# Performance work log

Measured on AMD Instinct MI355X. Metric: run time of the kernel, lower is better.

The kernel has to match this reference:

```python
import jax, jax.numpy as jnp
import numpy as np

Q_MAX = 127.0  # 2**(8-1) - 1

def _quant_per_tensor_absmax(t):
    # scale = clamp(absmax, 1e-5) / 127 ; q = round(t / scale)
    scale = jnp.maximum(jnp.max(jnp.abs(t)), 1e-5) / Q_MAX
    q = jnp.round(t / scale)
    return q, scale

def setup_inputs() -> dict:
    key = jax.random.key(0)
    k1, k2, k3 = jax.random.split(key, 3)
    B, S, IN, OUT = 4, 2048, 4096, 4096
    x = jax.random.normal(k1, (B, S, IN), dtype=jnp.float32)
    weight = jax.random.normal(k2, (OUT, IN), dtype=jnp.float32)
    bias = jax.random.normal(k3, (1, OUT), dtype=jnp.float32)
    return {"x": x, "weight": weight, "bias": bias}

def reference(x, weight, bias):
    # per-tensor weight quantization (done at from_float time in the original)
    q_w, s_w = _quant_per_tensor_absmax(weight)   # q_w: [OUT, IN] integer-valued
    # per-tensor activation quantization (forward path)
    q_x, s_x = _quant_per_tensor_absmax(x)        # q_x: [B, S, IN] integer-valued
    # int8 GEMM (simulated in fp32: values are small integers) + fused dequant
    y = jnp.einsum('bsi,oi->bso', q_x, q_w)       # [B, S, OUT]
    y = y * (s_x * s_w) + bias                    # dequant scale + bias
    return y
```

## Files before the change

### kernel.cpp

```cpp
#include <hip/hip_runtime.h>
#include <hip/hip_bf16.h>
#include <stdint.h>

#define M_DIM 8192
#define N_DIM 4096
#define K_DIM 4096

typedef int i32x4 __attribute__((ext_vector_type(4)));

#define NB_X 2048
#define NB_W 1024
#define NB_TOT (NB_X + NB_W)

__global__ void w8a8_absmax_kernel(const float* __restrict__ x,
                                   const float* __restrict__ w,
                                   float* __restrict__ partials) {
    int b = blockIdx.x;
    const float4* p;
    int n4, bi, nb;
    if (b < NB_X) { p = (const float4*)x; n4 = (M_DIM * K_DIM) / 4; bi = b;        nb = NB_X; }
    else          { p = (const float4*)w; n4 = (N_DIM * K_DIM) / 4; bi = b - NB_X; nb = NB_W; }

    float m = 0.f;
    int stride = nb * 256;
    for (int i = bi * 256 + threadIdx.x; i < n4; i += stride) {
        float4 v = p[i];
        m = fmaxf(m, fmaxf(fmaxf(fabsf(v.x), fabsf(v.y)), fmaxf(fabsf(v.z), fabsf(v.w))));
    }
    #pragma unroll
    for (int o = 32; o > 0; o >>= 1)
        m = fmaxf(m, __shfl_xor(m, o, 64));

    __shared__ float red[4];
    if ((threadIdx.x & 63) == 0) red[threadIdx.x >> 6] = m;
    __syncthreads();
    if (threadIdx.x == 0)
        partials[b] = fmaxf(fmaxf(red[0], red[1]), fmaxf(red[2], red[3]));
}

__global__ void w8a8_finalize_kernel(const float* __restrict__ partials,
                                     float* __restrict__ finals) {
    int base = (blockIdx.x == 0) ? 0 : NB_X;
    int n    = (blockIdx.x == 0) ? NB_X : NB_W;
    float m = 0.f;
    for (int i = threadIdx.x; i < n; i += 256)
        m = fmaxf(m, partials[base + i]);
    #pragma unroll
    for (int o = 32; o > 0; o >>= 1)
        m = fmaxf(m, __shfl_xor(m, o, 64));
    __shared__ float red[4];
    if ((threadIdx.x & 63) == 0) red[threadIdx.x >> 6] = m;
    __syncthreads();
    if (threadIdx.x == 0) {
        m = fmaxf(fmaxf(red[0], red[1]), fmaxf(red[2], red[3]));
        finals[blockIdx.x] = fmaxf(m, 1e-5f) / 127.0f;
    }
}

__global__ void w8a8_quant_kernel(const float* __restrict__ x,
                                  const float* __restrict__ w,
                                  unsigned* __restrict__ qx,
                                  unsigned* __restrict__ qw,
                                  const float* __restrict__ finals) {
    int b = blockIdx.x;
    const float4* in4;
    unsigned* outq;
    int n4, bi, nb;
    float scale;
    if (b < NB_X) { in4 = (const float4*)x; outq = qx; n4 = (M_DIM * K_DIM) / 4; bi = b;        nb = NB_X; scale = finals[0]; }
    else          { in4 = (const float4*)w; outq = qw; n4 = (N_DIM * K_DIM) / 4; bi = b - NB_X; nb = NB_W; scale = finals[1]; }

    int stride = nb * 256;
    for (int i = bi * 256 + threadIdx.x; i < n4; i += stride) {
        float4 v = in4[i];
        int q0 = (int)rintf(v.x / scale);
        int q1 = (int)rintf(v.y / scale);
        int q2 = (int)rintf(v.z / scale);
        int q3 = (int)rintf(v.w / scale);
        outq[i] = (unsigned)(q0 & 0xff) | ((unsigned)(q1 & 0xff) << 8) |
                  ((unsigned)(q2 & 0xff) << 16) | ((unsigned)(q3 & 0xff) << 24);
    }
}

#define BM 256
#define BN 256
#define BK 128
#define NT (K_DIM / BK)
#define NTN (N_DIM / BN)
#define LDS_BUF 65536

#define STAGE_A(BUF, MH, KT) do {                                              \
    _Pragma("unroll")                                                          \
    for (int r_ = 0; r_ < 2; ++r_)                                             \
        __builtin_amdgcn_global_load_lds(                                      \
            (const __attribute__((address_space(1))) void*)(a_base + (size_t)((KT) + goffA[MH][r_])), \
            (__attribute__((address_space(3))) void*)(lds + (BUF)*LDS_BUF + (MH)*16384 + ldst[r_]),   \
            16, 0, 0);                                                         \
} while (0)

#define STAGE_B(BUF, NH, KT) do {                                              \
    _Pragma("unroll")                                                          \
    for (int r_ = 0; r_ < 2; ++r_)                                             \
        __builtin_amdgcn_global_load_lds(                                      \
            (const __attribute__((address_space(1))) void*)(b_base + (size_t)((KT) + goffB[NH][r_])), \
            (__attribute__((address_space(3))) void*)(lds + (BUF)*LDS_BUF + 32768 + (NH)*16384 + ldst[r_]), \
            16, 0, 0);                                                         \
} while (0)

#define LOAD_A(BUF, MH) do {                                                   \
    _Pragma("unroll")                                                          \
    for (int m4_ = 0; m4_ < 4; ++m4_) {                                        \
        aF[m4_][0] = *(const i32x4*)(lds + (BUF)*LDS_BUF + (MH)*16384 + laneA + m4_*2048 + koff[0]); \
        aF[m4_][1] = *(const i32x4*)(lds + (BUF)*LDS_BUF + (MH)*16384 + laneA + m4_*2048 + koff[1]); \
    }                                                                          \
} while (0)

#define LOAD_B(BUF, NH) do {                                                   \
    _Pragma("unroll")                                                          \
    for (int n1_ = 0; n1_ < 2; ++n1_) {                                        \
        bF[n1_][0] = *(const i32x4*)(lds + (BUF)*LDS_BUF + 32768 + (NH)*16384 + laneB + n1_*2048 + koff[0]); \
        bF[n1_][1] = *(const i32x4*)(lds + (BUF)*LDS_BUF + 32768 + (NH)*16384 + laneB + n1_*2048 + koff[1]); \
    }                                                                          \
} while (0)

#define MMA(MH, NH) do {                                                       \
    __builtin_amdgcn_s_setprio(1);                                             \
    _Pragma("unroll")                                                          \
    for (int m4_ = 0; m4_ < 4; ++m4_) {                                        \
        _Pragma("unroll")                                                      \
        for (int n1_ = 0; n1_ < 2; ++n1_) {                                    \
            i32x4 c_ = acc[(MH)*4 + m4_][(NH)*2 + n1_];                        \
            c_ = __builtin_amdgcn_mfma_i32_16x16x64_i8(aF[m4_][0], bF[n1_][0], c_, 0, 0, 0); \
            c_ = __builtin_amdgcn_mfma_i32_16x16x64_i8(aF[m4_][1], bF[n1_][1], c_, 0, 0, 0); \
            acc[(MH)*4 + m4_][(NH)*2 + n1_] = c_;                              \
        }                                                                      \
    }                                                                          \
    __builtin_amdgcn_s_setprio(0);                                             \
} while (0)

#define BAR() __builtin_amdgcn_s_barrier()
#define VMW8() asm volatile("s_waitcnt vmcnt(8)" ::: "memory")

#define TILE_BODY(BUF, KT2) do {                                               \
    LOAD_A(BUF, 0); LOAD_B(BUF, 0);                         \
    BAR(); MMA(0, 0); BAR();                                                   \
    LOAD_A(BUF, 1);                                         \
    BAR(); MMA(1, 0); BAR();                                                   \
    LOAD_B(BUF, 1);                                         \
    STAGE_B(BUF, 0, KT2);                              \
    BAR(); MMA(1, 1); BAR();                                                   \
    LOAD_A(BUF, 0);                                         \
    STAGE_A(BUF, 1, KT2);                              \
    STAGE_B(BUF, 1, KT2);                              \
    BAR(); MMA(0, 1); BAR();                                                   \
    STAGE_A(BUF, 0, KT2);                              \
    VMW8();                                   \
    BAR();                                                                     \
} while (0)

__global__ __launch_bounds__(512, 2) void w8a8_gemm_kernel(
    const signed char* __restrict__ qa,
    const signed char* __restrict__ qb,
    const float* __restrict__ bias,
    const float* __restrict__ finals,
    float* __restrict__ out)
{
    __shared__ __align__(16) char lds[2 * LDS_BUF];

    int t    = threadIdx.x;
    int lane = t & 63;
    int wid  = t >> 6;
    int wm   = wid >> 2;
    int wn   = wid & 3;
    int fr   = lane & 15;
    int fg   = lane >> 4;
    int frb2 = (fr >> 2) & 1;

    int bid = blockIdx.x;
    int cpx = gridDim.x >> 3;
    int swz = (bid & 7) * cpx + (bid >> 3);
    int tm = swz / NTN;
    int tn = swz % NTN;

    const signed char* a_base = qa + (size_t)tm * BM * K_DIM;
    const signed char* b_base = qb + (size_t)tn * BN * K_DIM;

    int goffA[2][2], goffB[2][2], ldst[2];
    #pragma unroll
    for (int r = 0; r < 2; ++r) {
        int unit = r * 512 + t;
        int sl   = unit >> 3;
        int c    = unit & 7;
        int cs   = c ^ (sl & 7);
        int rowA = (sl & 63) + ((sl >> 6) & 1) * 128;
        goffA[0][r] = rowA * K_DIM + cs * 16;
        goffA[1][r] = (rowA + 64) * K_DIM + cs * 16;
        int rowB = ((sl >> 5) & 3) * 64 + (sl & 31);
        goffB[0][r] = rowB * K_DIM + cs * 16;
        goffB[1][r] = (rowB + 32) * K_DIM + cs * 16;
        ldst[r] = r * 8192 + t * 16;
    }

    int laneA = (wm * 64 + fr) * 128 + (fg ^ (fr & 3)) * 16;
    int laneB = (wn * 32 + fr) * 128 + (fg ^ (fr & 3)) * 16;
    int koff[2];
    koff[0] = frb2 * 64;
    koff[1] = 64 - frb2 * 64;

    i32x4 acc[8][4] = {};
    i32x4 aF[4][2], bF[2][2];

    STAGE_A(0, 0, 0);  STAGE_A(0, 1, 0);  STAGE_B(0, 0, 0);  STAGE_B(0, 1, 0);
    STAGE_A(1, 0, BK); STAGE_A(1, 1, BK); STAGE_B(1, 0, BK); STAGE_B(1, 1, BK);
    VMW8();
    BAR();

    #pragma unroll 1
    for (int it = 0; it < NT / 2; ++it) {
        int kt2 = ((2 * it + 2) & (NT - 1)) * BK;
        int kt3 = ((2 * it + 3) & (NT - 1)) * BK;
        TILE_BODY(0, kt2);
        TILE_BODY(1, kt3);
    }
    asm volatile("s_waitcnt vmcnt(0)" ::: "memory");
    BAR();

    float sprod = finals[0] * finals[1];
    int orow0 = tm * BM + wm * 128 + fg * 4;
    int ocol0 = tn * BN + wn * 64 + fr;
    #pragma unroll
    for (int n = 0; n < 4; ++n) {
        int col = ocol0 + n * 16;
        float bv = bias[col];
        #pragma unroll
        for (int m = 0; m < 8; ++m) {
            int row = orow0 + m * 16;
            #pragma unroll
            for (int rr = 0; rr < 4; ++rr) {
                out[(size_t)(row + rr) * N_DIM + col] = (float)acc[m][n][rr] * sprod + bv;
            }
        }
    }
}

extern "C" void kernel_launch(void* const* d_in, const int* in_sizes, int n_in,
                              void* d_out, int out_size, void* d_ws, size_t ws_size,
                              hipStream_t stream) {
    const float* x    = (const float*)d_in[0];
    const float* wgt  = (const float*)d_in[1];
    const float* bias = (const float*)d_in[2];
    float* out = (float*)d_out;

    char* ws = (char*)d_ws;
    float* finals   = (float*)ws;
    float* partials = (float*)(ws + 256);
    signed char* qx = (signed char*)(ws + 16384);
    signed char* qw = qx + (size_t)M_DIM * K_DIM;

    w8a8_absmax_kernel<<<NB_TOT, 256, 0, stream>>>(x, wgt, partials);
    w8a8_finalize_kernel<<<2, 256, 0, stream>>>(partials, finals);
    w8a8_quant_kernel<<<NB_TOT, 256, 0, stream>>>(x, wgt, (unsigned*)qx, (unsigned*)qw, finals);
    w8a8_gemm_kernel<<<(M_DIM / BM) * (N_DIM / BN), 512, 0, stream>>>(qx, qw, bias, finals, out);
}
```

Before: 226.4 us.

## Register double-buffer LDS fragments and reorder GEMM tile pipeline

The int8 GEMM main loop now keeps separate register fragments for the two A halves and for B. It ping-pongs the first B fragment across tiles and prefetches the next tile's first A/B fragments from the other LDS buffer during the last MMA group. Explicit lgkmcnt waits and sched_barriers replace the previous barrier pairs around each MMA block, so LDS reads can overlap with MFMA work and fewer barriers are needed. Launch bounds drop from 2 to 1 block per CU to make room for the extra registers, which risks lower occupancy and less latency hiding.

```diff
diff --git a/kernel.cpp b/kernel.cpp
--- a/kernel.cpp
+++ b/kernel.cpp
@@ -107,31 +107,31 @@
             16, 0, 0);                                                         \
 } while (0)
 
-#define LOAD_A(BUF, MH) do {                                                   \
+#define RA_A(BUF, MH, DST) do {                                                \
     _Pragma("unroll")                                                          \
     for (int m4_ = 0; m4_ < 4; ++m4_) {                                        \
-        aF[m4_][0] = *(const i32x4*)(lds + (BUF)*LDS_BUF + (MH)*16384 + laneA + m4_*2048 + koff[0]); \
-        aF[m4_][1] = *(const i32x4*)(lds + (BUF)*LDS_BUF + (MH)*16384 + laneA + m4_*2048 + koff[1]); \
+        DST[m4_][0] = *(const i32x4*)(lds + (BUF)*LDS_BUF + (MH)*16384 + laneA + m4_*2048 + koff[0]); \
+        DST[m4_][1] = *(const i32x4*)(lds + (BUF)*LDS_BUF + (MH)*16384 + laneA + m4_*2048 + koff[1]); \
     }                                                                          \
 } while (0)
 
-#define LOAD_B(BUF, NH) do {                                                   \
+#define RA_B(BUF, NH, DST) do {                                                \
     _Pragma("unroll")                                                          \
     for (int n1_ = 0; n1_ < 2; ++n1_) {                                        \
-        bF[n1_][0] = *(const i32x4*)(lds + (BUF)*LDS_BUF + 32768 + (NH)*16384 + laneB + n1_*2048 + koff[0]); \
-        bF[n1_][1] = *(const i32x4*)(lds + (BUF)*LDS_BUF + 32768 + (NH)*16384 + laneB + n1_*2048 + koff[1]); \
+        DST[n1_][0] = *(const i32x4*)(lds + (BUF)*LDS_BUF + 32768 + (NH)*16384 + laneB + n1_*2048 + koff[0]); \
+        DST[n1_][1] = *(const i32x4*)(lds + (BUF)*LDS_BUF + 32768 + (NH)*16384 + laneB + n1_*2048 + koff[1]); \
     }                                                                          \
 } while (0)
 
-#define MMA(MH, NH) do {                                                       \
+#define MMA4(MH, NH, AARR, BARR) do {                                          \
     __builtin_amdgcn_s_setprio(1);                                             \
     _Pragma("unroll")                                                          \
     for (int m4_ = 0; m4_ < 4; ++m4_) {                                        \
         _Pragma("unroll")                                                      \
         for (int n1_ = 0; n1_ < 2; ++n1_) {                                    \
             i32x4 c_ = acc[(MH)*4 + m4_][(NH)*2 + n1_];                        \
-            c_ = __builtin_amdgcn_mfma_i32_16x16x64_i8(aF[m4_][0], bF[n1_][0], c_, 0, 0, 0); \
-            c_ = __builtin_amdgcn_mfma_i32_16x16x64_i8(aF[m4_][1], bF[n1_][1], c_, 0, 0, 0); \
+            c_ = __builtin_amdgcn_mfma_i32_16x16x64_i8(AARR[m4_][0], BARR[n1_][0], c_, 0, 0, 0); \
+            c_ = __builtin_amdgcn_mfma_i32_16x16x64_i8(AARR[m4_][1], BARR[n1_][1], c_, 0, 0, 0); \
             acc[(MH)*4 + m4_][(NH)*2 + n1_] = c_;                              \
         }                                                                      \
     }                                                                          \
@@ -139,26 +139,38 @@
 } while (0)
 
 #define BAR() __builtin_amdgcn_s_barrier()
-#define VMW8() asm volatile("s_waitcnt vmcnt(8)" ::: "memory")
-
-#define TILE_BODY(BUF, KT2) do {                                               \
-    LOAD_A(BUF, 0); LOAD_B(BUF, 0);                         \
-    BAR(); MMA(0, 0); BAR();                                                   \
-    LOAD_A(BUF, 1);                                         \
-    BAR(); MMA(1, 0); BAR();                                                   \
-    LOAD_B(BUF, 1);                                         \
-    STAGE_B(BUF, 0, KT2);                              \
-    BAR(); MMA(1, 1); BAR();                                                   \
-    LOAD_A(BUF, 0);                                         \
-    STAGE_A(BUF, 1, KT2);                              \
-    STAGE_B(BUF, 1, KT2);                              \
-    BAR(); MMA(0, 1); BAR();                                                   \
-    STAGE_A(BUF, 0, KT2);                              \
-    VMW8();                                   \
-    BAR();                                                                     \
-} while (0)
-
-__global__ __launch_bounds__(512, 2) void w8a8_gemm_kernel(
+#define SB0() __builtin_amdgcn_sched_barrier(0)
+#define VMW(N) asm volatile("s_waitcnt vmcnt(" #N ")" ::: "memory")
+#define LGKM(N) asm volatile("s_waitcnt lgkmcnt(" #N ")" ::: "memory")
+
+#define TILE_BODY(BUF, OBUF, KT2, B0C, B0N) do {                               \
+                                              \
+    RA_B(BUF, 1, bB1);                                                         \
+    SB0(); LGKM(4); SB0();                         \
+    MMA4(0, 0, aA0, B0C);                                                      \
+    BAR();                                                                     \
+     \
+    STAGE_A(BUF, 0, KT2); STAGE_B(BUF, 0, KT2);                                \
+    RA_A(BUF, 1, aA1);                                                         \
+    SB0(); LGKM(8); SB0();                             \
+    MMA4(0, 1, aA0, bB1);                                                      \
+    BAR();                                                                     \
+                 \
+    STAGE_B(BUF, 1, KT2);                                                      \
+    SB0(); LGKM(0); SB0();                                        \
+    MMA4(1, 1, aA1, bB1);                                                      \
+    BAR();                                                                     \
+     \
+    VMW(6);                             \
+    BAR();                                \
+    RA_A(OBUF, 0, aA0); RA_B(OBUF, 0, B0N);                                    \
+    STAGE_A(BUF, 1, KT2);                                                      \
+    SB0();                                       \
+    MMA4(1, 0, aA1, B0C);                                                      \
+    BAR();                                                                     \
+} while (0)
+
+__global__ __launch_bounds__(512, 1) void w8a8_gemm_kernel(
     const signed char* __restrict__ qa,
     const signed char* __restrict__ qb,
     const float* __restrict__ bias,
@@ -208,21 +220,22 @@
     koff[1] = 64 - frb2 * 64;
 
     i32x4 acc[8][4] = {};
-    i32x4 aF[4][2], bF[2][2];
+    i32x4 aA0[4][2], aA1[4][2], bB1[2][2], bB0a[2][2], bB0b[2][2];
 
     STAGE_A(0, 0, 0);  STAGE_A(0, 1, 0);  STAGE_B(0, 0, 0);  STAGE_B(0, 1, 0);
     STAGE_A(1, 0, BK); STAGE_A(1, 1, BK); STAGE_B(1, 0, BK); STAGE_B(1, 1, BK);
-    VMW8();
+    VMW(8);
     BAR();
+    RA_A(0, 0, aA0); RA_B(0, 0, bB0a);
 
     #pragma unroll 1
     for (int it = 0; it < NT / 2; ++it) {
         int kt2 = ((2 * it + 2) & (NT - 1)) * BK;
         int kt3 = ((2 * it + 3) & (NT - 1)) * BK;
-        TILE_BODY(0, kt2);
-        TILE_BODY(1, kt3);
-    }
-    asm volatile("s_waitcnt vmcnt(0)" ::: "memory");
+        TILE_BODY(0, 1, kt2, bB0a, bB0b);
+        TILE_BODY(1, 0, kt3, bB0b, bB0a);
+    }
+    asm volatile("s_waitcnt vmcnt(0) lgkmcnt(0)" ::: "memory");
     BAR();
 
     float sprod = finals[0] * finals[1];
```

Result: faster. 217.9 us (-3.8%).
